# Performance work log

Hardware: AMD Instinct MI355X
Metric: run time of the kernel (lower is better)

Reference implementation:

```python
import jax, jax.numpy as jnp
import numpy as np

N_NODES = 100000
N_EDGES = 1600000
N_GRAPHS = 256
IN_C = 64
HID = 128
OUT = 128
BN_EPS = 1e-5


def setup_inputs() -> dict:
    key = jax.random.key(0)
    ks = jax.random.split(key, 24)
    x = jax.random.normal(ks[0], (N_NODES, IN_C), jnp.float32)
    edge_index = jax.random.randint(ks[1], (2, N_EDGES), 0, N_NODES, dtype=jnp.int64 if jax.config.jax_enable_x64 else jnp.int32)
    batch = jnp.sort(jax.random.randint(ks[2], (N_NODES,), 0, N_GRAPHS))

    def lin(k, i, o):
        return (jax.random.normal(k, (i, o), jnp.float32) / np.float32(np.sqrt(i)))

    d = {"x": x, "edge_index": edge_index, "batch": batch}
    in_dims = [IN_C, HID, HID]
    for l in range(3):
        d[f"w1_{l}"] = lin(ks[3 + 6 * l], in_dims[l], HID)
        d[f"b1_{l}"] = jnp.zeros((HID,), jnp.float32)
        d[f"w2_{l}"] = lin(ks[4 + 6 * l], HID, HID)
        d[f"b2_{l}"] = jnp.zeros((HID,), jnp.float32)
        d[f"gamma_{l}"] = jnp.ones((HID,), jnp.float32)
        d[f"beta_{l}"] = jnp.zeros((HID,), jnp.float32)
    d["proj_w"] = lin(ks[22], HID, OUT)
    d["proj_b"] = jnp.zeros((OUT,), jnp.float32)
    return d


def _gin_forward(x, edge_index, batch, layers, proj_w, proj_b):
    src, dst = edge_index[0], edge_index[1]
    h = x
    for (w1, b1, w2, b2, g, b) in layers:
        # GINConv (eps=0, aggr='add'): MLP(h_i + sum_{j->i} h_j)
        agg = jax.ops.segment_sum(h[src], dst, num_segments=h.shape[0])
        z = h + agg
        z = jax.nn.relu(z @ w1 + b1) @ w2 + b2
        # BatchNorm1d, training mode (biased batch stats)
        mean = z.mean(axis=0)
        var = z.var(axis=0)
        z = (z - mean) * jax.lax.rsqrt(var + BN_EPS) * g + b
        h = jax.nn.relu(z)
    # global_mean_pool over graph ids
    s = jax.ops.segment_sum(h, batch, num_segments=N_GRAPHS)
    cnt = jax.ops.segment_sum(jnp.ones((h.shape[0], 1), h.dtype), batch, num_segments=N_GRAPHS)
    hg = s / jnp.maximum(cnt, 1.0)
    return hg @ proj_w + proj_b


def reference(x, edge_index, batch,
              w1_0, b1_0, w2_0, b2_0, gamma_0, beta_0,
              w1_1, b1_1, w2_1, b2_1, gamma_1, beta_1,
              w1_2, b1_2, w2_2, b2_2, gamma_2, beta_2,
              proj_w, proj_b):
    layers = [
        (w1_0, b1_0, w2_0, b2_0, gamma_0, beta_0),
        (w1_1, b1_1, w2_1, b2_1, gamma_1, beta_1),
        (w1_2, b1_2, w2_2, b2_2, gamma_2, beta_2),
    ]
    return _gin_forward(x, edge_index, batch, layers, proj_w, proj_b)
```

## Files before the change

### kernel.cpp

```cpp
#include <hip/hip_runtime.h>

#define N_NODES 100000
#define N_EDGES 1600000
#define N_GRAPHS 256
#define HID 128
#define BN_EPS 1e-5f

#define NT 1563
#define EB 4096
#define RB 391
#define MB 1563

typedef __bf16 bf16x8 __attribute__((ext_vector_type(8)));
typedef __bf16 bf16x4 __attribute__((ext_vector_type(4)));
typedef __bf16 bf16x2 __attribute__((ext_vector_type(2)));
typedef float f32x4 __attribute__((ext_vector_type(4)));

__global__ __launch_bounds__(256) void prep_all_kernel(
    const float* __restrict__ wa, const float* __restrict__ wb,
    const float* __restrict__ wc, const float* __restrict__ wd,
    const float* __restrict__ we, const float* __restrict__ wf,
    __bf16* __restrict__ wt) {
  int idx = blockIdx.x * 256 + threadIdx.x;
  if (idx >= 90112) return;
  const float* w;
  int K, local;
  if (idx < 8192) { w = wa; K = 64; local = idx; }
  else {
    int s = (idx - 8192) / 16384;
    local = (idx - 8192) - s * 16384;
    K = 128;
    w = (s == 0) ? wb : (s == 1) ? wc : (s == 2) ? wd : (s == 3) ? we : wf;
  }
  int n = local / K, k = local - n * K;
  wt[idx] = (__bf16)w[k * 128 + n];
}

__global__ __launch_bounds__(256) void x_convert_kernel(const float* __restrict__ x,
                                                        __bf16* __restrict__ xb) {
  int idx = blockIdx.x * 256 + threadIdx.x;
  if (idx >= N_NODES * 16) return;
  f32x4 v = ((const f32x4*)x)[idx];
  bf16x4 o = {(__bf16)v[0], (__bf16)v[1], (__bf16)v[2], (__bf16)v[3]};
  ((bf16x4*)xb)[idx] = o;
}

__global__ __launch_bounds__(256) void tile_hist_kernel(const int* __restrict__ ei,
                                                        int* __restrict__ tcnt) {
  __shared__ int hist[NT];
  int t = threadIdx.x;
  for (int i = t; i < NT; i += 256) hist[i] = 0;
  __syncthreads();
  int base = blockIdx.x * EB;
#pragma unroll 4
  for (int i = 0; i < EB / 256; i++) {
    int e = base + i * 256 + t;
    if (e < N_EDGES) atomicAdd(&hist[ei[N_EDGES + e] >> 6], 1);
  }
  __syncthreads();
  for (int i = t; i < NT; i += 256) {
    int h = hist[i];
    if (h) atomicAdd(&tcnt[i], h);
  }
}

__global__ __launch_bounds__(256) void tile_scan_kernel(const int* __restrict__ tcnt,
                                                        int* __restrict__ tstart,
                                                        int* __restrict__ gcursor) {
  __shared__ int ps[256];
  int t = threadIdx.x;
  const int CH = (NT + 255) / 256;
  int lo = t * CH, hi = min(lo + CH, NT);
  int s = 0;
  for (int i = lo; i < hi; i++) s += tcnt[i];
  ps[t] = s;
  __syncthreads();
  for (int off = 1; off < 256; off <<= 1) {
    int v = ps[t];
    int u = (t >= off) ? ps[t - off] : 0;
    __syncthreads();
    ps[t] = v + u;
    __syncthreads();
  }
  int base = (t == 0) ? 0 : ps[t - 1];
  for (int i = lo; i < hi; i++) {
    tstart[i] = base;
    gcursor[i] = base;
    base += tcnt[i];
  }
  if (t == 0) tstart[NT] = N_EDGES;
}

__global__ __launch_bounds__(256) void reorder2_kernel(const int* __restrict__ ei,
                                                       int* __restrict__ gcursor,
                                                       int* __restrict__ epack) {
  __shared__ int hist[NT];
  int t = threadIdx.x;
  for (int i = t; i < NT; i += 256) hist[i] = 0;
  __syncthreads();
  int base = blockIdx.x * EB;
#pragma unroll 4
  for (int i = 0; i < EB / 256; i++) {
    int e = base + i * 256 + t;
    if (e < N_EDGES) atomicAdd(&hist[ei[N_EDGES + e] >> 6], 1);
  }
  __syncthreads();
  for (int i = t; i < NT; i += 256) {
    int h = hist[i];
    if (h) hist[i] = atomicAdd(&gcursor[i], h);
  }
  __syncthreads();
#pragma unroll 4
  for (int i = 0; i < EB / 256; i++) {
    int e = base + i * 256 + t;
    if (e < N_EDGES) {
      int d = ei[N_EDGES + e];
      int s = ei[e];
      int pos = atomicAdd(&hist[d >> 6], 1);
      epack[pos] = (s << 6) | (d & 63);
    }
  }
}

__global__ __launch_bounds__(256) void row_sort_kernel(const int* __restrict__ tstart,
                                                       const int* __restrict__ epack,
                                                       int* __restrict__ starts,
                                                       int* __restrict__ srcs) {
  __shared__ int cnt[64];
  __shared__ int rbase[65];
  __shared__ int rofs[64];
  int t = threadIdx.x, b = blockIdx.x;
  int ts = tstart[b], te = tstart[b + 1];
  if (t < 64) cnt[t] = 0;
  __syncthreads();
  for (int i = ts + t; i < te; i += 256) atomicAdd(&cnt[epack[i] & 63], 1);
  __syncthreads();
  if (t == 0) {
    int a = 0;
    for (int r = 0; r < 64; r++) { rbase[r] = a; a += cnt[r]; }
    rbase[64] = a;
  }
  __syncthreads();
  if (t < 64) rofs[t] = ts + rbase[t];
  if (t <= 64) {
    int gr = b * 64 + t;
    if (gr <= N_NODES) starts[gr] = ts + rbase[t];
  }
  __syncthreads();
  for (int i = ts + t; i < te; i += 256) {
    int p = epack[i];
    int pos = atomicAdd(&rofs[p & 63], 1);
    srcs[pos] = p >> 6;
  }
}

__global__ __launch_bounds__(256) void h_apply_kernel(const __bf16* __restrict__ u,
                                                      const float* __restrict__ bnab,
                                                      __bf16* __restrict__ h) {
  int idx = blockIdx.x * 256 + threadIdx.x;
  if (idx >= N_NODES * (HID / 8)) return;
  int c8 = idx & 15;
  bf16x8 v = ((const bf16x8*)u)[idx];
  f32x4 a0 = ((const f32x4*)bnab)[c8 * 2];
  f32x4 a1 = ((const f32x4*)bnab)[c8 * 2 + 1];
  f32x4 b0 = ((const f32x4*)(bnab + HID))[c8 * 2];
  f32x4 b1 = ((const f32x4*)(bnab + HID))[c8 * 2 + 1];
  bf16x8 o;
#pragma unroll
  for (int k = 0; k < 4; k++) {
    o[k] = (__bf16)fmaxf(fmaf(a0[k], (float)v[k], b0[k]), 0.f);
    o[4 + k] = (__bf16)fmaxf(fmaf(a1[k], (float)v[4 + k], b1[k]), 0.f);
  }
  ((bf16x8*)h)[idx] = o;
}

template <int C>
__global__ __launch_bounds__(256) void gather_kernel(const __bf16* __restrict__ h,
                                                     const int* __restrict__ starts,
                                                     const int* __restrict__ srcs,
                                                     __bf16* __restrict__ z) {
  const int lane = threadIdx.x & 63;
  const int row = blockIdx.x * 4 + (threadIdx.x >> 6);
  if (row >= N_NODES) return;
  int e0 = starts[row], e1 = starts[row + 1];
  int deg = e1 - e0;
  int idxv = srcs[min(e0 + lane, N_EDGES - 1)];
  int dcap = min(deg, 64);
  if constexpr (C == 64) {
    float acc = (float)h[(size_t)row * 64 + lane];
    float s0 = 0.f, s1 = 0.f, s2 = 0.f, s3 = 0.f, s4 = 0.f, s5 = 0.f, s6 = 0.f, s7 = 0.f;
    int j = 0;
    for (; j + 7 < dcap; j += 8) {
      int i0 = __builtin_amdgcn_readlane(idxv, j);
      int i1 = __builtin_amdgcn_readlane(idxv, j + 1);
      int i2 = __builtin_amdgcn_readlane(idxv, j + 2);
      int i3 = __builtin_amdgcn_readlane(idxv, j + 3);
      int i4 = __builtin_amdgcn_readlane(idxv, j + 4);
      int i5 = __builtin_amdgcn_readlane(idxv, j + 5);
      int i6 = __builtin_amdgcn_readlane(idxv, j + 6);
      int i7 = __builtin_amdgcn_readlane(idxv, j + 7);
      float v0 = (float)h[(size_t)i0 * 64 + lane];
      float v1 = (float)h[(size_t)i1 * 64 + lane];
      float v2 = (float)h[(size_t)i2 * 64 + lane];
      float v3 = (float)h[(size_t)i3 * 64 + lane];
      float v4 = (float)h[(size_t)i4 * 64 + lane];
      float v5 = (float)h[(size_t)i5 * 64 + lane];
      float v6 = (float)h[(size_t)i6 * 64 + lane];
      float v7 = (float)h[(size_t)i7 * 64 + lane];
      s0 += v0; s1 += v1; s2 += v2; s3 += v3;
      s4 += v4; s5 += v5; s6 += v6; s7 += v7;
    }
    for (; j < dcap; j++) {
      int i0 = __builtin_amdgcn_readlane(idxv, j);
      s0 += (float)h[(size_t)i0 * 64 + lane];
    }
    for (int e = e0 + 64; e < e1; e++) s0 += (float)h[(size_t)srcs[e] * 64 + lane];
    acc += ((s0 + s1) + (s2 + s3)) + ((s4 + s5) + (s6 + s7));
    z[(size_t)row * 64 + lane] = (__bf16)acc;
  } else {
    bf16x2 sv = *(const bf16x2*)(h + (size_t)row * 128 + lane * 2);
    float ax = (float)sv[0], ay = (float)sv[1];
    float2 s0 = {0.f, 0.f}, s1 = {0.f, 0.f}, s2 = {0.f, 0.f}, s3 = {0.f, 0.f};
    float2 s4 = {0.f, 0.f}, s5 = {0.f, 0.f}, s6 = {0.f, 0.f}, s7 = {0.f, 0.f};
    int j = 0;
    for (; j + 7 < dcap; j += 8) {
      int i0 = __builtin_amdgcn_readlane(idxv, j);
      int i1 = __builtin_amdgcn_readlane(idxv, j + 1);
      int i2 = __builtin_amdgcn_readlane(idxv, j + 2);
      int i3 = __builtin_amdgcn_readlane(idxv, j + 3);
      int i4 = __builtin_amdgcn_readlane(idxv, j + 4);
      int i5 = __builtin_amdgcn_readlane(idxv, j + 5);
      int i6 = __builtin_amdgcn_readlane(idxv, j + 6);
      int i7 = __builtin_amdgcn_readlane(idxv, j + 7);
      bf16x2 v0 = *(const bf16x2*)(h + (size_t)i0 * 128 + lane * 2);
      bf16x2 v1 = *(const bf16x2*)(h + (size_t)i1 * 128 + lane * 2);
      bf16x2 v2 = *(const bf16x2*)(h + (size_t)i2 * 128 + lane * 2);
      bf16x2 v3 = *(const bf16x2*)(h + (size_t)i3 * 128 + lane * 2);
      bf16x2 v4 = *(const bf16x2*)(h + (size_t)i4 * 128 + lane * 2);
      bf16x2 v5 = *(const bf16x2*)(h + (size_t)i5 * 128 + lane * 2);
      bf16x2 v6 = *(const bf16x2*)(h + (size_t)i6 * 128 + lane * 2);
      bf16x2 v7 = *(const bf16x2*)(h + (size_t)i7 * 128 + lane * 2);
      s0.x += (float)v0[0]; s0.y += (float)v0[1];
      s1.x += (float)v1[0]; s1.y += (float)v1[1];
      s2.x += (float)v2[0]; s2.y += (float)v2[1];
      s3.x += (float)v3[0]; s3.y += (float)v3[1];
      s4.x += (float)v4[0]; s4.y += (float)v4[1];
      s5.x += (float)v5[0]; s5.y += (float)v5[1];
      s6.x += (float)v6[0]; s6.y += (float)v6[1];
      s7.x += (float)v7[0]; s7.y += (float)v7[1];
    }
    for (; j < dcap; j++) {
      int i0 = __builtin_amdgcn_readlane(idxv, j);
      bf16x2 vv = *(const bf16x2*)(h + (size_t)i0 * 128 + lane * 2);
      s0.x += (float)vv[0]; s0.y += (float)vv[1];
    }
    for (int e = e0 + 64; e < e1; e++) {
      bf16x2 vv = *(const bf16x2*)(h + (size_t)srcs[e] * 128 + lane * 2);
      s0.x += (float)vv[0]; s0.y += (float)vv[1];
    }
    ax += ((s0.x + s1.x) + (s2.x + s3.x)) + ((s4.x + s5.x) + (s6.x + s7.x));
    ay += ((s0.y + s1.y) + (s2.y + s3.y)) + ((s4.y + s5.y) + (s6.y + s7.y));
    bf16x2 z2 = {(__bf16)ax, (__bf16)ay};
    *(bf16x2*)(z + (size_t)row * 128 + lane * 2) = z2;
  }
}

template <int CIN>
__global__ __launch_bounds__(256, 4) void mlp_kernel(
    const __bf16* __restrict__ z, const __bf16* __restrict__ w1t,
    const float* __restrict__ b1, const __bf16* __restrict__ w2t,
    const float* __restrict__ b2, __bf16* __restrict__ u,
    float* __restrict__ part) {
  constexpr int ZS = CIN + 8;
  constexpr int TS = HID + 8;
  constexpr int ZB = 64 * ZS * 2;
  constexpr int TB = 64 * TS * 2;
  constexpr int SB = (CIN == 128) ? TB : (ZB + TB);
  __shared__ __align__(16) char smem[SB];
  __bf16* zt = (__bf16*)smem;
  __bf16* tt = (CIN == 128) ? (__bf16*)smem : (__bf16*)(smem + ZB);

  const int t = threadIdx.x;
  const int wave = t >> 6;
  const int lane = t & 63;
  const int l16 = lane & 15;
  const int quad = lane >> 4;
  const int rowbase = blockIdx.x * 64;
  const int nvalid = min(64, N_NODES - rowbase);

  {
    constexpr int CH = CIN / 8;
    const bf16x8 zero8 = {};
    for (int f = t; f < 64 * CH; f += 256) {
      int r = f / CH, c = f - r * CH;
      int gr = rowbase + r;
      bf16x8 v = (gr < N_NODES) ? *(const bf16x8*)(z + (size_t)gr * CIN + c * 8) : zero8;
      *(bf16x8*)(zt + r * ZS + c * 8) = v;
    }
  }
  __syncthreads();

  const f32x4 zero4 = {0.f, 0.f, 0.f, 0.f};
  f32x4 acc[8];

  {
#pragma unroll
    for (int ct = 0; ct < 8; ct++) acc[ct] = zero4;
    const __bf16* arow = zt + (wave * 16 + l16) * ZS + quad * 8;
#pragma unroll
    for (int ks = 0; ks < CIN / 32; ks++) {
      bf16x8 af = *(const bf16x8*)(arow + ks * 32);
#pragma unroll
      for (int ct = 0; ct < 8; ct++) {
        bf16x8 bfr = *(const bf16x8*)(w1t + (ct * 16 + l16) * CIN + ks * 32 + quad * 8);
        acc[ct] = __builtin_amdgcn_mfma_f32_16x16x32_bf16(af, bfr, acc[ct], 0, 0, 0);
      }
    }
#pragma unroll
    for (int ct = 0; ct < 8; ct++) {
      int col = ct * 16 + l16;
      float bias = b1[col];
#pragma unroll
      for (int r = 0; r < 4; r++) {
        float v = acc[ct][r] + bias;
        tt[(wave * 16 + quad * 4 + r) * TS + col] = (__bf16)(v > 0.f ? v : 0.f);
      }
    }
  }

  {
#pragma unroll
    for (int ct = 0; ct < 8; ct++) acc[ct] = zero4;
    const __bf16* arow = tt + (wave * 16 + l16) * TS + quad * 8;
#pragma unroll
    for (int ks = 0; ks < HID / 32; ks++) {
      bf16x8 af = *(const bf16x8*)(arow + ks * 32);
#pragma unroll
      for (int ct = 0; ct < 8; ct++) {
        bf16x8 bfr = *(const bf16x8*)(w2t + (ct * 16 + l16) * HID + ks * 32 + quad * 8);
        acc[ct] = __builtin_amdgcn_mfma_f32_16x16x32_bf16(af, bfr, acc[ct], 0, 0, 0);
      }
    }
#pragma unroll
    for (int ct = 0; ct < 8; ct++) {
      int col = ct * 16 + l16;
      float bias = b2[col];
#pragma unroll
      for (int r = 0; r < 4; r++) {
        tt[(wave * 16 + quad * 4 + r) * TS + col] = (__bf16)(acc[ct][r] + bias);
      }
    }
  }
  __syncthreads();

  for (int f = t; f < 64 * 16; f += 256) {
    int r = f >> 4, c = f & 15;
    if (r < nvalid) {
      bf16x8 v = *(const bf16x8*)(tt + r * TS + c * 8);
      *(bf16x8*)(u + (size_t)(rowbase + r) * HID + c * 8) = v;
    }
  }
  if (t < HID) {
    float s = 0.f, sq = 0.f;
    for (int r = 0; r < nvalid; r++) {
      float v = (float)tt[r * TS + t];
      s += v;
      sq += v * v;
    }
    part[(size_t)blockIdx.x * 256 + t] = s;
    part[(size_t)blockIdx.x * 256 + HID + t] = sq;
  }
}

__global__ __launch_bounds__(256) void bn_stats_kernel(const float* __restrict__ part,
                                                       const float* __restrict__ gamma,
                                                       const float* __restrict__ beta,
                                                       float* __restrict__ bnab) {
  __shared__ float ss[256], qq[256];
  int c = blockIdx.x;
  int t = threadIdx.x;
  float s = 0.f, q = 0.f;
  for (int b = t; b < MB; b += 256) {
    s += part[(size_t)b * 256 + c];
    q += part[(size_t)b * 256 + HID + c];
  }
  ss[t] = s; qq[t] = q;
  __syncthreads();
  for (int off = 128; off > 0; off >>= 1) {
    if (t < off) { ss[t] += ss[t + off]; qq[t] += qq[t + off]; }
    __syncthreads();
  }
  if (t == 0) {
    const float invN = 1.f / (float)N_NODES;
    float mean = ss[0] * invN;
    float var = qq[0] * invN - mean * mean;
    float a = gamma[c] * rsqrtf(var + BN_EPS);
    bnab[c] = a;
    bnab[HID + c] = beta[c] - mean * a;
  }
}

__global__ __launch_bounds__(128) void bn_apply_pool_kernel(const __bf16* __restrict__ u,
                                                            const float* __restrict__ bnab,
                                                            const int* __restrict__ batch,
                                                            float* __restrict__ pool) {
  int c = threadIdx.x;
  int r0 = blockIdx.x * 64;
  if (r0 >= N_NODES) return;
  int rend = min(r0 + 64, N_NODES);
  float a = bnab[c], b = bnab[HID + c];
  float accv = 0.f;
  int curg = -1;
  for (int r = r0; r < rend; r++) {
    int g = batch[r];
    if (g != curg) {
      if (curg >= 0) atomicAdd(&pool[curg * HID + c], accv);
      curg = g;
      accv = 0.f;
    }
    float v = (float)u[(size_t)r * HID + c];
    v = v * a + b;
    accv += (v > 0.f ? v : 0.f);
  }
  if (curg >= 0) atomicAdd(&pool[curg * HID + c], accv);
}

__global__ __launch_bounds__(256) void count_kernel(const int* __restrict__ batch,
                                                    int* __restrict__ counts) {
  int t = blockIdx.x * 256 + threadIdx.x;
  int r0 = t * 64;
  if (r0 >= N_NODES) return;
  int rend = min(r0 + 64, N_NODES);
  int curg = batch[r0], cnt = 0;
  for (int r = r0; r < rend; r++) {
    int g = batch[r];
    if (g != curg) {
      atomicAdd(&counts[curg], cnt);
      curg = g;
      cnt = 1;
    } else {
      cnt++;
    }
  }
  atomicAdd(&counts[curg], cnt);
}

__global__ __launch_bounds__(128) void pool_proj_kernel(const float* __restrict__ pool,
                                                        const int* __restrict__ counts,
                                                        const float* __restrict__ pw,
                                                        const float* __restrict__ pb,
                                                        float* __restrict__ out) {
  int g = blockIdx.x;
  int c = threadIdx.x;
  __shared__ float hg[HID];
  float cnt = (float)max(counts[g], 1);
  hg[c] = pool[g * HID + c] / cnt;
  __syncthreads();
  float acc = pb[c];
#pragma unroll 8
  for (int k = 0; k < HID; k++) acc += hg[k] * pw[k * HID + c];
  out[g * HID + c] = acc;
}

extern "C" void kernel_launch(void* const* d_in, const int* in_sizes, int n_in,
                              void* d_out, int out_size, void* d_ws, size_t ws_size,
                              hipStream_t stream) {
  (void)in_sizes; (void)n_in; (void)out_size; (void)ws_size;
  const float* x = (const float*)d_in[0];
  const int* ei = (const int*)d_in[1];
  const int* batch = (const int*)d_in[2];
  const float* w1[3] = {(const float*)d_in[3], (const float*)d_in[9], (const float*)d_in[15]};
  const float* b1[3] = {(const float*)d_in[4], (const float*)d_in[10], (const float*)d_in[16]};
  const float* w2[3] = {(const float*)d_in[5], (const float*)d_in[11], (const float*)d_in[17]};
  const float* b2[3] = {(const float*)d_in[6], (const float*)d_in[12], (const float*)d_in[18]};
  const float* gm[3] = {(const float*)d_in[7], (const float*)d_in[13], (const float*)d_in[19]};
  const float* bt[3] = {(const float*)d_in[8], (const float*)d_in[14], (const float*)d_in[20]};
  const float* pw = (const float*)d_in[21];
  const float* pb = (const float*)d_in[22];
  float* out = (float*)d_out;

  char* ws = (char*)d_ws;
  __bf16* bufA = (__bf16*)ws;        ws += (size_t)N_NODES * HID * 2;
  __bf16* bufB = (__bf16*)ws;        ws += (size_t)N_NODES * HID * 2;
  __bf16* bufC = (__bf16*)ws;        ws += (size_t)N_NODES * HID * 2;
  __bf16* z0 = (__bf16*)ws;          ws += (size_t)N_NODES * 64 * 2;
  __bf16* xb = (__bf16*)ws;          ws += (size_t)N_NODES * 64 * 2;
  int* srcs = (int*)ws;              ws += (size_t)N_EDGES * 4;
  int* epack = (int*)ws;             ws += (size_t)N_EDGES * 4;
  int* starts = (int*)ws;            ws += (size_t)(N_NODES + 1) * 4;
  int* tcnt = (int*)ws;              ws += NT * 4;
  int* tstart = (int*)ws;            ws += (NT + 1) * 4;
  int* gcursor = (int*)ws;           ws += NT * 4;
  ws = (char*)(((uintptr_t)ws + 63) & ~(uintptr_t)63);
  float* part = (float*)ws;          ws += (size_t)MB * 256 * 4;
  __bf16* wt_all = (__bf16*)ws;      ws += 90112 * 2;
  ws = (char*)(((uintptr_t)ws + 63) & ~(uintptr_t)63);
  float* bnab = (float*)ws;          ws += 256 * 4;
  float* pool = (float*)ws;          ws += N_GRAPHS * HID * 4;
  int* counts = (int*)ws;            ws += N_GRAPHS * 4;

  __bf16* w1t0 = wt_all;
  __bf16* w2t0 = wt_all + 8192;
  __bf16* w1t1 = wt_all + 24576;
  __bf16* w2t1 = wt_all + 40960;
  __bf16* w1t2 = wt_all + 57344;
  __bf16* w2t2 = wt_all + 73728;

  const int mlp_blocks = MB;
  const int gat_blocks = (N_NODES + 3) / 4;
  const int app_blocks = (N_NODES * (HID / 8) + 255) / 256;

  prep_all_kernel<<<(90112 + 255) / 256, 256, 0, stream>>>(
      w1[0], w2[0], w1[1], w2[1], w1[2], w2[2], wt_all);
  x_convert_kernel<<<(N_NODES * 16 + 255) / 256, 256, 0, stream>>>(x, xb);

  hipMemsetAsync(tcnt, 0, NT * 4, stream);
  tile_hist_kernel<<<RB, 256, 0, stream>>>(ei, tcnt);
  tile_scan_kernel<<<1, 256, 0, stream>>>(tcnt, tstart, gcursor);
  reorder2_kernel<<<RB, 256, 0, stream>>>(ei, gcursor, epack);
  row_sort_kernel<<<NT, 256, 0, stream>>>(tstart, epack, starts, srcs);

  hipMemsetAsync(pool, 0, (size_t)N_GRAPHS * HID * 4 + N_GRAPHS * 4, stream);
  count_kernel<<<((N_NODES + 63) / 64 + 255) / 256, 256, 0, stream>>>(batch, counts);

  gather_kernel<64><<<gat_blocks, 256, 0, stream>>>(xb, starts, srcs, z0);
  mlp_kernel<64><<<mlp_blocks, 256, 0, stream>>>(z0, w1t0, b1[0], w2t0, b2[0], bufA, part);
  bn_stats_kernel<<<HID, 256, 0, stream>>>(part, gm[0], bt[0], bnab);

  h_apply_kernel<<<app_blocks, 256, 0, stream>>>(bufA, bnab, bufB);
  gather_kernel<128><<<gat_blocks, 256, 0, stream>>>(bufB, starts, srcs, bufC);
  mlp_kernel<128><<<mlp_blocks, 256, 0, stream>>>(bufC, w1t1, b1[1], w2t1, b2[1], bufC, part);
  bn_stats_kernel<<<HID, 256, 0, stream>>>(part, gm[1], bt[1], bnab);

  h_apply_kernel<<<app_blocks, 256, 0, stream>>>(bufC, bnab, bufA);
  gather_kernel<128><<<gat_blocks, 256, 0, stream>>>(bufA, starts, srcs, bufB);
  mlp_kernel<128><<<mlp_blocks, 256, 0, stream>>>(bufB, w1t2, b1[2], w2t2, b2[2], bufB, part);
  bn_stats_kernel<<<HID, 256, 0, stream>>>(part, gm[2], bt[2], bnab);

  bn_apply_pool_kernel<<<mlp_blocks, 128, 0, stream>>>(bufB, bnab, batch, pool);

  pool_proj_kernel<<<N_GRAPHS, 128, 0, stream>>>(pool, counts, pw, pb, out);
}
```

Baseline: 611.3 us.

## Process two row tiles per MLP block with register prefetch of next tile

The MLP kernel now handles two 64-row tiles per block. While the current tile is being computed, the next tile's input is loaded into registers so global-load latency overlaps with the MFMA work. Per-column BN partial statistics are split across all 256 threads, two halves per tile, and the partial buffer and reduction length grow to match. Outputs are written out of place into separate buffers, one of which reuses the z0/xb region. This halves the grid to 782 blocks, which reduces occupancy and parallelism on a large GPU and adds register pressure from the staging buffer.

```diff
diff --git a/kernel.cpp b/kernel.cpp
--- a/kernel.cpp
+++ b/kernel.cpp
@@ -9,7 +9,9 @@
 #define NT 1563
 #define EB 4096
 #define RB 391
-#define MB 1563
+#define MTILES 1564
+#define MBLK 782
+#define PARTN 3128
 
 typedef __bf16 bf16x8 __attribute__((ext_vector_type(8)));
 typedef __bf16 bf16x4 __attribute__((ext_vector_type(4)));
@@ -276,99 +278,127 @@
   constexpr int ZB = 64 * ZS * 2;
   constexpr int TB = 64 * TS * 2;
   constexpr int SB = (CIN == 128) ? TB : (ZB + TB);
+  constexpr int CH = CIN / 8;
+  constexpr int NLD = 64 * CH / 256;
+  constexpr int TILES = 2;
   __shared__ __align__(16) char smem[SB];
   __bf16* zt = (__bf16*)smem;
   __bf16* tt = (CIN == 128) ? (__bf16*)smem : (__bf16*)(smem + ZB);
 
   const int t = threadIdx.x;
   const int wave = t >> 6;
-  const int lane = t & 63;
-  const int l16 = lane & 15;
-  const int quad = lane >> 4;
-  const int rowbase = blockIdx.x * 64;
-  const int nvalid = min(64, N_NODES - rowbase);
+  const int l16 = t & 15;
+  const int quad = (t & 63) >> 4;
+  const f32x4 zero4 = {0.f, 0.f, 0.f, 0.f};
+  const bf16x8 zero8 = {};
+
+  const int tile0 = blockIdx.x * TILES;
+  bf16x8 stg[NLD];
 
   {
-    constexpr int CH = CIN / 8;
-    const bf16x8 zero8 = {};
-    for (int f = t; f < 64 * CH; f += 256) {
+    int rowbase = tile0 * 64;
+#pragma unroll
+    for (int n = 0; n < NLD; n++) {
+      int f = t + n * 256;
       int r = f / CH, c = f - r * CH;
       int gr = rowbase + r;
-      bf16x8 v = (gr < N_NODES) ? *(const bf16x8*)(z + (size_t)gr * CIN + c * 8) : zero8;
-      *(bf16x8*)(zt + r * ZS + c * 8) = v;
-    }
-  }
-  __syncthreads();
-
-  const f32x4 zero4 = {0.f, 0.f, 0.f, 0.f};
-  f32x4 acc[8];
-
-  {
-#pragma unroll
-    for (int ct = 0; ct < 8; ct++) acc[ct] = zero4;
-    const __bf16* arow = zt + (wave * 16 + l16) * ZS + quad * 8;
-#pragma unroll
-    for (int ks = 0; ks < CIN / 32; ks++) {
-      bf16x8 af = *(const bf16x8*)(arow + ks * 32);
+      stg[n] = (gr < N_NODES) ? *(const bf16x8*)(z + (size_t)gr * CIN + c * 8) : zero8;
+    }
+  }
+
+#pragma unroll
+  for (int it = 0; it < TILES; it++) {
+    const int rowbase = (tile0 + it) * 64;
+    const int nvalid = min(64, max(0, N_NODES - rowbase));
+    __syncthreads();
+#pragma unroll
+    for (int n = 0; n < NLD; n++) {
+      int f = t + n * 256;
+      int r = f / CH, c = f - r * CH;
+      *(bf16x8*)(zt + r * ZS + c * 8) = stg[n];
+    }
+    __syncthreads();
+    if (it + 1 < TILES) {
+      int rb2 = (tile0 + it + 1) * 64;
+#pragma unroll
+      for (int n = 0; n < NLD; n++) {
+        int f = t + n * 256;
+        int r = f / CH, c = f - r * CH;
+        int gr = rb2 + r;
+        stg[n] = (gr < N_NODES) ? *(const bf16x8*)(z + (size_t)gr * CIN + c * 8) : zero8;
+      }
+    }
+
+    f32x4 acc[8];
+    {
+#pragma unroll
+      for (int ct = 0; ct < 8; ct++) acc[ct] = zero4;
+      const __bf16* arow = zt + (wave * 16 + l16) * ZS + quad * 8;
+#pragma unroll
+      for (int ks = 0; ks < CIN / 32; ks++) {
+        bf16x8 af = *(const bf16x8*)(arow + ks * 32);
+#pragma unroll
+        for (int ct = 0; ct < 8; ct++) {
+          bf16x8 bfr = *(const bf16x8*)(w1t + (ct * 16 + l16) * CIN + ks * 32 + quad * 8);
+          acc[ct] = __builtin_amdgcn_mfma_f32_16x16x32_bf16(af, bfr, acc[ct], 0, 0, 0);
+        }
+      }
 #pragma unroll
       for (int ct = 0; ct < 8; ct++) {
-        bf16x8 bfr = *(const bf16x8*)(w1t + (ct * 16 + l16) * CIN + ks * 32 + quad * 8);
-        acc[ct] = __builtin_amdgcn_mfma_f32_16x16x32_bf16(af, bfr, acc[ct], 0, 0, 0);
-      }
-    }
-#pragma unroll
-    for (int ct = 0; ct < 8; ct++) {
-      int col = ct * 16 + l16;
-      float bias = b1[col];
-#pragma unroll
-      for (int r = 0; r < 4; r++) {
-        float v = acc[ct][r] + bias;
-        tt[(wave * 16 + quad * 4 + r) * TS + col] = (__bf16)(v > 0.f ? v : 0.f);
-      }
-    }
-  }
-
-  {
-#pragma unroll
-    for (int ct = 0; ct < 8; ct++) acc[ct] = zero4;
-    const __bf16* arow = tt + (wave * 16 + l16) * TS + quad * 8;
-#pragma unroll
-    for (int ks = 0; ks < HID / 32; ks++) {
-      bf16x8 af = *(const bf16x8*)(arow + ks * 32);
+        int col = ct * 16 + l16;
+        float bias = b1[col];
+#pragma unroll
+        for (int r = 0; r < 4; r++) {
+          float v = acc[ct][r] + bias;
+          tt[(wave * 16 + quad * 4 + r) * TS + col] = (__bf16)(v > 0.f ? v : 0.f);
+        }
+      }
+    }
+    {
+#pragma unroll
+      for (int ct = 0; ct < 8; ct++) acc[ct] = zero4;
+      const __bf16* arow = tt + (wave * 16 + l16) * TS + quad * 8;
+#pragma unroll
+      for (int ks = 0; ks < HID / 32; ks++) {
+        bf16x8 af = *(const bf16x8*)(arow + ks * 32);
+#pragma unroll
+        for (int ct = 0; ct < 8; ct++) {
+          bf16x8 bfr = *(const bf16x8*)(w2t + (ct * 16 + l16) * HID + ks * 32 + quad * 8);
+          acc[ct] = __builtin_amdgcn_mfma_f32_16x16x32_bf16(af, bfr, acc[ct], 0, 0, 0);
+        }
+      }
 #pragma unroll
       for (int ct = 0; ct < 8; ct++) {
-        bf16x8 bfr = *(const bf16x8*)(w2t + (ct * 16 + l16) * HID + ks * 32 + quad * 8);
-        acc[ct] = __builtin_amdgcn_mfma_f32_16x16x32_bf16(af, bfr, acc[ct], 0, 0, 0);
-      }
-    }
-#pragma unroll
-    for (int ct = 0; ct < 8; ct++) {
-      int col = ct * 16 + l16;
-      float bias = b2[col];
-#pragma unroll
-      for (int r = 0; r < 4; r++) {
-        tt[(wave * 16 + quad * 4 + r) * TS + col] = (__bf16)(acc[ct][r] + bias);
-      }
-    }
-  }
-  __syncthreads();
-
-  for (int f = t; f < 64 * 16; f += 256) {
-    int r = f >> 4, c = f & 15;
-    if (r < nvalid) {
-      bf16x8 v = *(const bf16x8*)(tt + r * TS + c * 8);
-      *(bf16x8*)(u + (size_t)(rowbase + r) * HID + c * 8) = v;
-    }
-  }
-  if (t < HID) {
-    float s = 0.f, sq = 0.f;
-    for (int r = 0; r < nvalid; r++) {
-      float v = (float)tt[r * TS + t];
-      s += v;
-      sq += v * v;
-    }
-    part[(size_t)blockIdx.x * 256 + t] = s;
-    part[(size_t)blockIdx.x * 256 + HID + t] = sq;
+        int col = ct * 16 + l16;
+        float bias = b2[col];
+#pragma unroll
+        for (int r = 0; r < 4; r++) {
+          tt[(wave * 16 + quad * 4 + r) * TS + col] = (__bf16)(acc[ct][r] + bias);
+        }
+      }
+    }
+    __syncthreads();
+
+    for (int f = t; f < 64 * 16; f += 256) {
+      int r = f >> 4, c = f & 15;
+      if (r < nvalid) {
+        bf16x8 v = *(const bf16x8*)(tt + r * TS + c * 8);
+        *(bf16x8*)(u + (size_t)(rowbase + r) * HID + c * 8) = v;
+      }
+    }
+    {
+      int col = t & 127, half = t >> 7;
+      int r0 = half * 32, r1 = min(r0 + 32, nvalid);
+      float s = 0.f, sq = 0.f;
+      for (int r = r0; r < r1; r++) {
+        float v = (float)tt[r * TS + col];
+        s += v;
+        sq += v * v;
+      }
+      size_t pb = ((size_t)(tile0 + it) * 2 + half) * 256;
+      part[pb + col] = s;
+      part[pb + HID + col] = sq;
+    }
   }
 }
 
@@ -380,7 +410,7 @@
   int c = blockIdx.x;
   int t = threadIdx.x;
   float s = 0.f, q = 0.f;
-  for (int b = t; b < MB; b += 256) {
+  for (int b = t; b < PARTN; b += 256) {
     s += part[(size_t)b * 256 + c];
     q += part[(size_t)b * 256 + HID + c];
   }
@@ -485,6 +515,7 @@
   __bf16* bufC = (__bf16*)ws;        ws += (size_t)N_NODES * HID * 2;
   __bf16* z0 = (__bf16*)ws;          ws += (size_t)N_NODES * 64 * 2;
   __bf16* xb = (__bf16*)ws;          ws += (size_t)N_NODES * 64 * 2;
+  __bf16* bufD = z0;
   int* srcs = (int*)ws;              ws += (size_t)N_EDGES * 4;
   int* epack = (int*)ws;             ws += (size_t)N_EDGES * 4;
   int* starts = (int*)ws;            ws += (size_t)(N_NODES + 1) * 4;
@@ -492,7 +523,7 @@
   int* tstart = (int*)ws;            ws += (NT + 1) * 4;
   int* gcursor = (int*)ws;           ws += NT * 4;
   ws = (char*)(((uintptr_t)ws + 63) & ~(uintptr_t)63);
-  float* part = (float*)ws;          ws += (size_t)MB * 256 * 4;
+  float* part = (float*)ws;          ws += (size_t)PARTN * 256 * 4;
   __bf16* wt_all = (__bf16*)ws;      ws += 90112 * 2;
   ws = (char*)(((uintptr_t)ws + 63) & ~(uintptr_t)63);
   float* bnab = (float*)ws;          ws += 256 * 4;
@@ -506,7 +537,6 @@
   __bf16* w1t2 = wt_all + 57344;
   __bf16* w2t2 = wt_all + 73728;
 
-  const int mlp_blocks = MB;
   const int gat_blocks = (N_NODES + 3) / 4;
   const int app_blocks = (N_NODES * (HID / 8) + 255) / 256;
 
@@ -524,20 +554,20 @@
   count_kernel<<<((N_NODES + 63) / 64 + 255) / 256, 256, 0, stream>>>(batch, counts);
 
   gather_kernel<64><<<gat_blocks, 256, 0, stream>>>(xb, starts, srcs, z0);
-  mlp_kernel<64><<<mlp_blocks, 256, 0, stream>>>(z0, w1t0, b1[0], w2t0, b2[0], bufA, part);
+  mlp_kernel<64><<<MBLK, 256, 0, stream>>>(z0, w1t0, b1[0], w2t0, b2[0], bufA, part);
   bn_stats_kernel<<<HID, 256, 0, stream>>>(part, gm[0], bt[0], bnab);
 
   h_apply_kernel<<<app_blocks, 256, 0, stream>>>(bufA, bnab, bufB);
   gather_kernel<128><<<gat_blocks, 256, 0, stream>>>(bufB, starts, srcs, bufC);
-  mlp_kernel<128><<<mlp_blocks, 256, 0, stream>>>(bufC, w1t1, b1[1], w2t1, b2[1], bufC, part);
+  mlp_kernel<128><<<MBLK, 256, 0, stream>>>(bufC, w1t1, b1[1], w2t1, b2[1], bufD, part);
   bn_stats_kernel<<<HID, 256, 0, stream>>>(part, gm[1], bt[1], bnab);
 
-  h_apply_kernel<<<app_blocks, 256, 0, stream>>>(bufC, bnab, bufA);
+  h_apply_kernel<<<app_blocks, 256, 0, stream>>>(bufD, bnab, bufA);
   gather_kernel<128><<<gat_blocks, 256, 0, stream>>>(bufA, starts, srcs, bufB);
-  mlp_kernel<128><<<mlp_blocks, 256, 0, stream>>>(bufB, w1t2, b1[2], w2t2, b2[2], bufB, part);
+  mlp_kernel<128><<<MBLK, 256, 0, stream>>>(bufB, w1t2, b1[2], w2t2, b2[2], bufC, part);
   bn_stats_kernel<<<HID, 256, 0, stream>>>(part, gm[2], bt[2], bnab);
 
-  bn_apply_pool_kernel<<<mlp_blocks, 128, 0, stream>>>(bufB, bnab, batch, pool);
+  bn_apply_pool_kernel<<<(N_NODES + 63) / 64, 128, 0, stream>>>(bufC, bnab, batch, pool);
 
   pool_proj_kernel<<<N_GRAPHS, 128, 0, stream>>>(pool, counts, pw, pb, out);
 }
```

Result: slower. 674.4 us (+10.3%).
